# Kernel optimization log

Measured on AMD Instinct MI355X. Metric: run time of the kernel, lower is better.

The kernel has to match this reference:

```python
import jax, jax.numpy as jnp
import numpy as np

UNITS = 80
LATENT = 128
IN_DIM = 256
BATCH = 8192
SIZE = 256


def _lstm_zero_state_step(x, K, b):
    """One Keras LSTM step from zero (h0, c0). activation=relu, recurrent_activation=sigmoid.
    With h0=0 the recurrent kernel contributes nothing; with c0=0 the forget gate is inert.
    Keras gate order in kernel/bias: i, f, c, o."""
    z = x @ K + b                       # (B, 4*UNITS)
    zi, zf, zc, zo = jnp.split(z, 4, axis=-1)
    c = jax.nn.sigmoid(zi) * jax.nn.relu(zc)   # i * act(c_tilde)
    return jax.nn.sigmoid(zo) * jax.nn.relu(c) # o * act(c)


def setup_inputs() -> dict:
    key = jax.random.key(0)
    ks = jax.random.split(key, 9)
    s = 0.05
    return {
        "x": jax.random.normal(ks[0], (BATCH, IN_DIM), jnp.float32),
        "size": SIZE,
        "W_lat": jax.random.normal(ks[1], (IN_DIM, LATENT), jnp.float32) * s,
        "b_lat": jax.random.normal(ks[2], (LATENT,), jnp.float32) * s,
        "K_fw": jax.random.normal(ks[3], (LATENT, 4 * UNITS), jnp.float32) * s,
        "b_fw": jax.random.normal(ks[4], (4 * UNITS,), jnp.float32) * s,
        "K_bw": jax.random.normal(ks[5], (LATENT, 4 * UNITS), jnp.float32) * s,
        "b_bw": jax.random.normal(ks[6], (4 * UNITS,), jnp.float32) * s,
        "K_1": jax.random.normal(ks[7], (2 * UNITS, 4 * UNITS), jnp.float32) * s,
        "b_1": jax.random.normal(ks[8], (4 * UNITS,), jnp.float32) * s,
    }


def reference(x, size, W_lat, b_lat, K_fw, b_fw, K_bw, b_bw, K_1, b_1):
    # Dense latent projection
    lat = x @ W_lat + b_lat                      # (B, 128)

    def decode_step(inp):                        # inp: (B, 128)
        # Bidirectional over a length-1 sequence: fw and bw both see the same
        # single timestep; merge mode is concat([forward, backward]).
        h_fw = _lstm_zero_state_step(inp, K_fw, b_fw)
        h_bw = _lstm_zero_state_step(inp, K_bw, b_bw)
        h = jnp.concatenate([h_fw, h_bw], axis=-1)   # (B, 160)
        return _lstm_zero_state_step(h, K_1, b_1)    # (B, 80)

    # The original Python loop feeds the latent vector only on iteration 0;
    # every later iteration feeds tf.ones(x_shape), and all Keras layers are
    # stateless (fresh zero state each call), so steps 1..size-1 are identical.
    y0 = decode_step(lat)                         # (B, 80)
    yc = decode_step(jnp.ones_like(lat))          # (B, 80)
    B = x.shape[0]
    rest = jnp.broadcast_to(yc[:, None, :], (B, size - 1, UNITS))
    return jnp.concatenate([y0[:, None, :], rest], axis=1)  # (B, size, 80)
```

## Files before the change

### kernel.cpp

```cpp
#include <hip/hip_runtime.h>
#include <math.h>

#define UNITS 80
#define LATENT 128
#define IN_DIM 256
#define BATCH 8192
#define SEQ 256
#define G 320
#define H2 160
#define ROW_F4 (SEQ * UNITS / 4)

#define TPB 640
#define RPB 8
#define NBLK (BATCH / RPB)

typedef float f4 __attribute__((ext_vector_type(4)));

__device__ __forceinline__ float sigf(float v) {
    return 1.0f / (1.0f + __expf(-v));
}

__global__ __launch_bounds__(TPB)
void main_kernel(const float* __restrict__ x,
                 const float* __restrict__ Wl, const float* __restrict__ bl,
                 const float* __restrict__ Kf, const float* __restrict__ bf,
                 const float* __restrict__ Kb, const float* __restrict__ bb,
                 const float* __restrict__ K1, const float* __restrict__ b1,
                 float* __restrict__ out) {
    __shared__ float z2[2 * G];
    __shared__ float h_c[H2];
    __shared__ float yc_s[UNITS];
    __shared__ float xs[RPB * IN_DIM];
    __shared__ float lat_s[RPB * LATENT];
    __shared__ float h_s[RPB * H2];
    __shared__ float y_s[RPB * UNITS];

    const int t = threadIdx.x;
    const int R0 = blockIdx.x * RPB;

    if (t < RPB * IN_DIM / 4)
        ((f4*)xs)[t] = ((const f4*)(x + (size_t)R0 * IN_DIM))[t];

    {
        const float* K   = (t < G) ? Kf : Kb;
        const float* bia = (t < G) ? bf : bb;
        const int c = (t < G) ? t : t - G;
        float acc = bia[c];
#pragma unroll 8
        for (int l = 0; l < LATENT; ++l) acc += K[l * G + c];
        z2[t] = acc;
    }
    __syncthreads();

    if (t < UNITS) {
        h_c[t] = sigf(z2[240 + t]) * sigf(z2[t]) * fmaxf(z2[160 + t], 0.f);
    } else if (t >= G && t < G + UNITS) {
        const int u = t - G;
        h_c[UNITS + u] = sigf(z2[G + 240 + u]) * sigf(z2[G + u]) * fmaxf(z2[G + 160 + u], 0.f);
    }
    __syncthreads();

    if (t < G) {
        float acc = b1[t];
#pragma unroll 8
        for (int l = 0; l < H2; ++l) acc = fmaf(h_c[l], K1[l * G + t], acc);
        z2[t] = acc;
    }
    __syncthreads();
    if (t < UNITS) yc_s[t] = sigf(z2[240 + t]) * sigf(z2[t]) * fmaxf(z2[160 + t], 0.f);
    __syncthreads();

    if (t < 512) {
        const int col = t & 127;
        const int rg  = t >> 7;
        float a0 = bl[col], a1 = a0;
        const float* xr0 = xs + (2 * rg) * IN_DIM;
        const float* xr1 = xr0 + IN_DIM;
#pragma unroll 4
        for (int l = 0; l < IN_DIM; ++l) {
            const float w = Wl[l * LATENT + col];
            a0 = fmaf(xr0[l], w, a0);
            a1 = fmaf(xr1[l], w, a1);
        }
        lat_s[(2 * rg) * LATENT + col] = a0;
        lat_s[(2 * rg + 1) * LATENT + col] = a1;
    }
    __syncthreads();

    if (t < 2 * G / 2) {
        const int u = t % UNITS;
        const int g = t / UNITS;
        const int half = g >> 1;
        const int r0 = (g & 1) * 4;
        const float* K   = half ? Kb : Kf;
        const float* bia = half ? bb : bf;
        float ai[4], ac[4], ao[4];
#pragma unroll
        for (int r = 0; r < 4; ++r) { ai[r] = bia[u]; ac[r] = bia[160 + u]; ao[r] = bia[240 + u]; }
#pragma unroll 2
        for (int k = 0; k < LATENT; ++k) {
            const float wi = K[k * G + u];
            const float wc = K[k * G + 160 + u];
            const float wo = K[k * G + 240 + u];
#pragma unroll
            for (int r = 0; r < 4; ++r) {
                const float lv = lat_s[(r0 + r) * LATENT + k];
                ai[r] = fmaf(lv, wi, ai[r]);
                ac[r] = fmaf(lv, wc, ac[r]);
                ao[r] = fmaf(lv, wo, ao[r]);
            }
        }
#pragma unroll
        for (int r = 0; r < 4; ++r)
            h_s[(r0 + r) * H2 + half * UNITS + u] =
                sigf(ao[r]) * sigf(ai[r]) * fmaxf(ac[r], 0.f);
    }
    __syncthreads();

    if (t < 2 * UNITS) {
        const int u = t % UNITS;
        const int g = t / UNITS;
        const int r0 = g * 4;
        float ai[4], ac[4], ao[4];
#pragma unroll
        for (int r = 0; r < 4; ++r) { ai[r] = b1[u]; ac[r] = b1[160 + u]; ao[r] = b1[240 + u]; }
#pragma unroll 2
        for (int k = 0; k < H2; ++k) {
            const float wi = K1[k * G + u];
            const float wc = K1[k * G + 160 + u];
            const float wo = K1[k * G + 240 + u];
#pragma unroll
            for (int r = 0; r < 4; ++r) {
                const float hv = h_s[(r0 + r) * H2 + k];
                ai[r] = fmaf(hv, wi, ai[r]);
                ac[r] = fmaf(hv, wc, ac[r]);
                ao[r] = fmaf(hv, wo, ao[r]);
            }
        }
#pragma unroll
        for (int r = 0; r < 4; ++r)
            y_s[(r0 + r) * UNITS + u] = sigf(ao[r]) * sigf(ai[r]) * fmaxf(ac[r], 0.f);
    }
    __syncthreads();

    __builtin_amdgcn_sched_barrier(0);

    {
        const f4 yv = ((const f4*)yc_s)[t % (UNITS / 4)];
        const f4* ys4 = (const f4*)y_s;
        f4* out4 = (f4*)out;
#pragma unroll
        for (int r = 0; r < RPB; ++r) {
            f4* rowp = out4 + (size_t)(R0 + r) * ROW_F4;
            const f4 v0 = (t < UNITS / 4) ? ys4[r * (UNITS / 4) + t] : yv;
            __builtin_nontemporal_store(v0, rowp + t);
#pragma unroll
            for (int k = 1; k < ROW_F4 / TPB; ++k)
                __builtin_nontemporal_store(yv, rowp + t + k * TPB);
        }
    }
}

extern "C" void kernel_launch(void* const* d_in, const int* in_sizes, int n_in,
                              void* d_out, int out_size, void* d_ws, size_t ws_size,
                              hipStream_t stream) {
    const float* x   = (const float*)d_in[0];
    const float* Wl  = (const float*)d_in[2];
    const float* bl  = (const float*)d_in[3];
    const float* Kf  = (const float*)d_in[4];
    const float* bf  = (const float*)d_in[5];
    const float* Kb  = (const float*)d_in[6];
    const float* bb  = (const float*)d_in[7];
    const float* K1  = (const float*)d_in[8];
    const float* b1  = (const float*)d_in[9];
    float* out = (float*)d_out;

    main_kernel<<<NBLK, TPB, 0, stream>>>(x, Wl, bl, Kf, bf, Kb, bb, K1, b1, out);
}
```

Measured before the change: 184.8 us.

## Split broadcast fill into separate grid-stride kernel after compute kernel

The compute kernel now writes only the first timestep row per batch element and stores the constant step vector to workspace. A second small-grid kernel (260x256 threads) does the bulk broadcast fill with a grid-stride loop using regular stores. The bulk write no longer has to wait on each block's per-row compute, and fewer persistent waves stream the output. In exchange it adds a second launch, and the fill uses plain stores instead of nontemporal ones. The stride of 66560 f4 is a multiple of the row length of 5120 f4, so each thread's column stays fixed across the loop. That is what lets each thread load the constant once.

Result: slower. 261.5 us (+41.5%).

```diff
diff --git a/kernel.cpp b/kernel.cpp
--- a/kernel.cpp
+++ b/kernel.cpp
@@ -9,10 +9,15 @@
 #define G 320
 #define H2 160
 #define ROW_F4 (SEQ * UNITS / 4)
+#define TOT_F4 ((long long)BATCH * ROW_F4)
 
 #define TPB 640
 #define RPB 8
 #define NBLK (BATCH / RPB)
+
+#define WB2 260
+#define WT2 256
+#define WSTRIDE2 (WB2 * WT2)
 
 typedef float f4 __attribute__((ext_vector_type(4)));
 
@@ -21,12 +26,12 @@
 }
 
 __global__ __launch_bounds__(TPB)
-void main_kernel(const float* __restrict__ x,
-                 const float* __restrict__ Wl, const float* __restrict__ bl,
-                 const float* __restrict__ Kf, const float* __restrict__ bf,
-                 const float* __restrict__ Kb, const float* __restrict__ bb,
-                 const float* __restrict__ K1, const float* __restrict__ b1,
-                 float* __restrict__ out) {
+void compute_kernel(const float* __restrict__ x,
+                    const float* __restrict__ Wl, const float* __restrict__ bl,
+                    const float* __restrict__ Kf, const float* __restrict__ bf,
+                    const float* __restrict__ Kb, const float* __restrict__ bb,
+                    const float* __restrict__ K1, const float* __restrict__ b1,
+                    float* __restrict__ yc, float* __restrict__ out) {
     __shared__ float z2[2 * G];
     __shared__ float h_c[H2];
     __shared__ float yc_s[UNITS];
@@ -68,7 +73,6 @@
     }
     __syncthreads();
     if (t < UNITS) yc_s[t] = sigf(z2[240 + t]) * sigf(z2[t]) * fmaxf(z2[160 + t], 0.f);
-    __syncthreads();
 
     if (t < 512) {
         const int col = t & 127;
@@ -87,7 +91,7 @@
     }
     __syncthreads();
 
-    if (t < 2 * G / 2) {
+    if (t < G) {
         const int u = t % UNITS;
         const int g = t / UNITS;
         const int half = g >> 1;
@@ -146,19 +150,26 @@
     __builtin_amdgcn_sched_barrier(0);
 
     {
-        const f4 yv = ((const f4*)yc_s)[t % (UNITS / 4)];
         const f4* ys4 = (const f4*)y_s;
         f4* out4 = (f4*)out;
-#pragma unroll
-        for (int r = 0; r < RPB; ++r) {
-            f4* rowp = out4 + (size_t)(R0 + r) * ROW_F4;
-            const f4 v0 = (t < UNITS / 4) ? ys4[r * (UNITS / 4) + t] : yv;
-            __builtin_nontemporal_store(v0, rowp + t);
-#pragma unroll
-            for (int k = 1; k < ROW_F4 / TPB; ++k)
-                __builtin_nontemporal_store(yv, rowp + t + k * TPB);
+        if (t < RPB * (UNITS / 4)) {
+            const int row = t / (UNITS / 4);
+            const int q = t - row * (UNITS / 4);
+            __builtin_nontemporal_store(ys4[t], out4 + (size_t)(R0 + row) * ROW_F4 + q);
         }
+        if (blockIdx.x == 0 && t < UNITS) yc[t] = yc_s[t];
     }
+}
+
+__global__ __launch_bounds__(WT2)
+void body_kernel(const float* __restrict__ yc, float* __restrict__ out) {
+    const long long g0 = (long long)blockIdx.x * WT2 + threadIdx.x;
+    const int c = (int)(g0 % ROW_F4);
+    if (c < UNITS / 4) return;
+    const f4 yv = ((const f4*)yc)[c % (UNITS / 4)];
+    f4* out4 = (f4*)out;
+    for (long long g = g0; g < TOT_F4; g += WSTRIDE2)
+        out4[g] = yv;
 }
 
 extern "C" void kernel_launch(void* const* d_in, const int* in_sizes, int n_in,
@@ -174,6 +185,8 @@
     const float* K1  = (const float*)d_in[8];
     const float* b1  = (const float*)d_in[9];
     float* out = (float*)d_out;
+    float* yc  = (float*)d_ws;
 
-    main_kernel<<<NBLK, TPB, 0, stream>>>(x, Wl, bl, Kf, bf, Kb, bb, K1, b1, out);
+    compute_kernel<<<NBLK, TPB, 0, stream>>>(x, Wl, bl, Kf, bf, Kb, bb, K1, b1, yc, out);
+    body_kernel<<<WB2, WT2, 0, stream>>>(yc, out);
 }
```
